# Optimization experiments

Measured on AMD Instinct MI355X. Metric: run time of the kernel, lower is better.

Reference implementation:

```python
import jax, jax.numpy as jnp
import numpy as np

N_NODES = 20000
N_EDGES = 320000
L = 128
NODE_IN = 30
EDGE_IN = 4
NUM_LAYERS = 5


def _mlp(x, w1, b1, a, w2, b2):
    # Linear -> PReLU(scalar slope) -> Linear
    h = x @ w1 + b1
    h = jnp.where(h > 0, h, a * h)
    return h @ w2 + b2


def setup_inputs() -> dict:
    key = jax.random.key(0)
    ks = iter(jax.random.split(key, 64))
    s = 0.02

    def w(shape):
        return (s * jax.random.normal(next(ks), shape)).astype(jnp.float32)

    inp = {}
    inp["x"] = jax.random.normal(next(ks), (N_NODES, NODE_IN), dtype=jnp.float32)
    inp["edge_attr"] = jax.random.normal(next(ks), (N_EDGES, EDGE_IN), dtype=jnp.float32)
    inp["edge_index"] = jax.random.randint(next(ks), (2, N_EDGES), 0, N_NODES, dtype=jnp.int32)
    # node encoder
    inp["ne_w1"] = w((NODE_IN, L)); inp["ne_b1"] = jnp.zeros((L,), jnp.float32)
    inp["ne_a"] = jnp.float32(0.25)
    inp["ne_w2"] = w((L, L)); inp["ne_b2"] = jnp.zeros((L,), jnp.float32)
    # edge encoder
    inp["ee_w1"] = w((EDGE_IN, L)); inp["ee_b1"] = jnp.zeros((L,), jnp.float32)
    inp["ee_a"] = jnp.float32(0.25)
    inp["ee_w2"] = w((L, L)); inp["ee_b2"] = jnp.zeros((L,), jnp.float32)
    # processor layers (stacked over NUM_LAYERS)
    inp["le_w1"] = w((NUM_LAYERS, 3 * L, L)); inp["le_b1"] = jnp.zeros((NUM_LAYERS, L), jnp.float32)
    inp["le_a"] = jnp.full((NUM_LAYERS,), 0.25, jnp.float32)
    inp["le_w2"] = w((NUM_LAYERS, L, L)); inp["le_b2"] = jnp.zeros((NUM_LAYERS, L), jnp.float32)
    inp["ln_w1"] = w((NUM_LAYERS, 2 * L, L)); inp["ln_b1"] = jnp.zeros((NUM_LAYERS, L), jnp.float32)
    inp["ln_a"] = jnp.full((NUM_LAYERS,), 0.25, jnp.float32)
    inp["ln_w2"] = w((NUM_LAYERS, L, L)); inp["ln_b2"] = jnp.zeros((NUM_LAYERS, L), jnp.float32)
    # decoder
    inp["de_w1"] = w((L, L)); inp["de_b1"] = jnp.zeros((L,), jnp.float32)
    inp["de_a"] = jnp.float32(0.25)
    inp["de_w2"] = w((L, 3)); inp["de_b2"] = jnp.zeros((3,), jnp.float32)
    return inp


def reference(x, edge_attr, edge_index,
              ne_w1, ne_b1, ne_a, ne_w2, ne_b2,
              ee_w1, ee_b1, ee_a, ee_w2, ee_b2,
              le_w1, le_b1, le_a, le_w2, le_b2,
              ln_w1, ln_b1, ln_a, ln_w2, ln_b2,
              de_w1, de_b1, de_a, de_w2, de_b2):
    n = x.shape[0]
    src = edge_index[0]  # x_j (source)
    dst = edge_index[1]  # x_i (target), aggregation index

    h = _mlp(x, ne_w1, ne_b1, ne_a, ne_w2, ne_b2)            # [N, L]
    e = _mlp(edge_attr, ee_w1, ee_b1, ee_a, ee_w2, ee_b2)    # [E, L]

    for l in range(le_w1.shape[0]):
        m = jnp.concatenate([h[dst], h[src], e], axis=-1)    # [E, 3L]
        m = _mlp(m, le_w1[l], le_b1[l], le_a[l], le_w2[l], le_b2[l])  # [E, L]
        agg = jax.ops.segment_sum(m, dst, num_segments=n)    # [N, L]
        upd = _mlp(jnp.concatenate([h, agg], axis=-1),
                   ln_w1[l], ln_b1[l], ln_a[l], ln_w2[l], ln_b2[l])
        h = h + upd

    return _mlp(h, de_w1, de_b1, de_a, de_w2, de_b2)         # [N, 3]
```

## Files before the change

### kernel.cpp

```cpp
#include <hip/hip_runtime.h>
#include <cstdint>
#include <cstddef>


#define DEVI static __device__ __forceinline__

typedef __bf16 bf16_t;
typedef bf16_t bf16x8 __attribute__((ext_vector_type(8)));
typedef bf16_t bf16x4 __attribute__((ext_vector_type(4)));
typedef float f32x4v __attribute__((ext_vector_type(4)));

DEVI float4 ld4(const float* p) { return *(const float4*)p; }
DEVI void st4(float* p, float4 v) { *(float4*)p = v; }
DEVI float prelu1(float z, float a) { return z > 0.f ? z : a * z; }
DEVI void atomicAddF(float* p, float v) {
  __hip_atomic_fetch_add(p, v, __ATOMIC_RELAXED, __HIP_MEMORY_SCOPE_AGENT);
}
DEVI f32x4v mfma_bf16(bf16x8 a, bf16x8 b, f32x4v c) {
  return __builtin_amdgcn_mfma_f32_16x16x32_bf16(a, b, c, 0, 0, 0);
}
DEVI void mfma3(f32x4v& acc, bf16x8 ah, bf16x8 al, bf16x8 bh, bf16x8 bl) {
  acc = mfma_bf16(ah, bh, acc);
  acc = mfma_bf16(al, bh, acc);
  acc = mfma_bf16(ah, bl, acc);
}
DEVI void split2(float x, bf16_t& h, bf16_t& l) {
  h = (bf16_t)x;
  l = (bf16_t)(x - (float)h);
}
DEVI bf16x8 ldb8(const bf16_t* p) { return *(const bf16x8*)p; }

#define NST 136
#define EST 72


DEVI void stage_f32(const float* __restrict__ src, int row0, int M,
                    int lane, int wave, bf16_t* SAh, bf16_t* SAl)
{
  const int row = wave * 16 + (lane >> 2);
  const int grow = row0 + row;
  const int colbase = (lane & 3) * 32;
  #pragma unroll
  for (int j = 0; j < 8; ++j) {
    int kc = colbase + j * 4;
    float4 v = make_float4(0.f, 0.f, 0.f, 0.f);
    if (grow < M) v = ld4(src + (size_t)grow * 128 + kc);
    bf16_t h0,l0,h1,l1,h2,l2,h3,l3;
    split2(v.x,h0,l0); split2(v.y,h1,l1); split2(v.z,h2,l2); split2(v.w,h3,l3);
    *(bf16x4*)(SAh + row * NST + kc) = (bf16x4){h0,h1,h2,h3};
    *(bf16x4*)(SAl + row * NST + kc) = (bf16x4){l0,l1,l2,l3};
  }
}

DEVI void stage_planes(const bf16_t* __restrict__ gh, const bf16_t* __restrict__ gl,
                       int row0, int M, int lane, int wave,
                       bf16_t* SAh, bf16_t* SAl)
{
  const int row = wave * 16 + (lane >> 2);
  const int grow = row0 + row;
  const int colbase = (lane & 3) * 32;
  #pragma unroll
  for (int j = 0; j < 4; ++j) {
    int kc = colbase + j * 8;
    bf16x8 vh = {};
    bf16x8 vl = {};
    if (grow < M) {
      vh = ldb8(gh + (size_t)grow * 128 + kc);
      vl = ldb8(gl + (size_t)grow * 128 + kc);
    }
    *(bf16x8*)(SAh + row * NST + kc) = vh;
    *(bf16x8*)(SAl + row * NST + kc) = vl;
  }
}

DEVI void gemm_lds(const bf16_t* SAh, const bf16_t* SAl,
                   const bf16_t* __restrict__ BT, f32x4v acc[8],
                   int wave, int p, int q)
{
  #pragma unroll
  for (int ks = 0; ks < 4; ++ks) {
    const int k0 = ks * 32 + q * 8;
    bf16x8 aH = ldb8(SAh + (wave * 16 + p) * NST + k0);
    bf16x8 aL = ldb8(SAl + (wave * 16 + p) * NST + k0);
    #pragma unroll
    for (int nt = 0; nt < 8; ++nt) {
      const bf16_t* bp = BT + (size_t)(nt * 16 + p) * 128 + k0;
      mfma3(acc[nt], aH, aL, ldb8(bp), ldb8(bp + 16384));
    }
  }
}

DEVI void store_c(float* __restrict__ O, int row0, int M,
                  const f32x4v acc[8], int wave, int p, int q)
{
  int rb = row0 + wave * 16 + q * 4;
  #pragma unroll
  for (int r = 0; r < 4; ++r) {
    if (rb + r < M) {
      float* op = O + (size_t)(rb + r) * 128 + p * 8;
      st4(op,     make_float4(acc[0][r], acc[1][r], acc[2][r], acc[3][r]));
      st4(op + 4, make_float4(acc[4][r], acc[5][r], acc[6][r], acc[7][r]));
    }
  }
}

DEVI void stage_cregs(const f32x4v acc[8], int wave, int p, int q,
                      bf16_t* SAh, bf16_t* SAl)
{
  #pragma unroll
  for (int r = 0; r < 4; ++r) {
    int row = wave * 16 + q * 4 + r;
    bf16x8 vh, vl;
    #pragma unroll
    for (int nt = 0; nt < 8; ++nt) {
      bf16_t hb, lb;
      split2(acc[nt][r], hb, lb);
      vh[nt] = hb; vl[nt] = lb;
    }
    *(bf16x8*)(SAh + row * NST + p * 8) = vh;
    *(bf16x8*)(SAl + row * NST + p * 8) = vl;
  }
}

DEVI void planes_out(bf16_t* __restrict__ gh, bf16_t* __restrict__ gl,
                     int row0, int M, int lane, int wave,
                     const bf16_t* SAh, const bf16_t* SAl)
{
  const int row = wave * 16 + (lane >> 2);
  const int grow = row0 + row;
  const int colbase = (lane & 3) * 32;
  if (grow < M) {
    #pragma unroll
    for (int j = 0; j < 4; ++j) {
      int kc = colbase + j * 8;
      *(bf16x8*)(gh + (size_t)grow * 128 + kc) = *(const bf16x8*)(SAh + row * NST + kc);
      *(bf16x8*)(gl + (size_t)grow * 128 + kc) = *(const bf16x8*)(SAl + row * NST + kc);
    }
  }
}

DEVI void ld8f(float dst[8], const float* __restrict__ src, int p) {
  *(float4*)(dst)     = ld4(src + p * 8);
  *(float4*)(dst + 4) = ld4(src + p * 8 + 4);
}

__global__ __launch_bounds__(128, 2) void k_svu(
    float* Sbuf,
    bf16_t* __restrict__ hSh, bf16_t* __restrict__ hSl,
    const bf16_t* __restrict__ WtilT, const bf16_t* __restrict__ Wn1aT,
    const bf16_t* __restrict__ lnw2T, const bf16_t* __restrict__ W1nextT,
    const float* __restrict__ ln_b1_l, const float* __restrict__ btil_l,
    const int* __restrict__ deg, const float* __restrict__ ln_a_l,
    const float* __restrict__ ln_b2_l,
    float* __restrict__ P, float* __restrict__ Q, int doPQ, int M)
{
  __shared__ __align__(16) bf16_t SAh[32 * NST];
  __shared__ __align__(16) bf16_t SAl[32 * NST];
  const int t = threadIdx.x, lane = t & 63, wave = t >> 6;
  const int p = lane & 15, q = lane >> 4;
  const int row0 = blockIdx.x * 32;

  f32x4v acc1[8];
  #pragma unroll
  for (int j = 0; j < 8; ++j) acc1[j] = (f32x4v){0.f, 0.f, 0.f, 0.f};

  stage_f32(Sbuf, row0, M, lane, wave, SAh, SAl);
  {
    const int row = wave * 16 + (lane >> 2);
    const int grow = row0 + row;
    const int colbase = (lane & 3) * 32;
    if (grow < M) {
      float4 z4 = make_float4(0.f, 0.f, 0.f, 0.f);
      #pragma unroll
      for (int j = 0; j < 8; ++j)
        st4(Sbuf + (size_t)grow * 128 + colbase + j * 4, z4);
    }
  }
  gemm_lds(SAh, SAl, WtilT, acc1, wave, p, q);
  stage_planes(hSh, hSl, row0, M, lane, wave, SAh, SAl);
  gemm_lds(SAh, SAl, Wn1aT, acc1, wave, p, q);

  float hold[8][4];
  #pragma unroll
  for (int r = 0; r < 4; ++r) {
    int row = wave * 16 + q * 4 + r;
    bf16x8 vh = *(const bf16x8*)(SAh + row * NST + p * 8);
    bf16x8 vl = *(const bf16x8*)(SAl + row * NST + p * 8);
    #pragma unroll
    for (int nt = 0; nt < 8; ++nt)
      hold[nt][r] = (float)vh[nt] + (float)vl[nt];
  }
  const float alpha = *ln_a_l;
  float degf[4];
  #pragma unroll
  for (int r = 0; r < 4; ++r) {
    int row = row0 + wave * 16 + q * 4 + r;
    degf[r] = (row < M) ? (float)deg[row] : 0.f;
  }
  float b1c[8], btc[8];
  ld8f(b1c, ln_b1_l, p);
  ld8f(btc, btil_l, p);
  #pragma unroll
  for (int nt = 0; nt < 8; ++nt)
    #pragma unroll
    for (int r = 0; r < 4; ++r)
      acc1[nt][r] = prelu1(acc1[nt][r] + b1c[nt] + degf[r] * btc[nt], alpha);

  stage_cregs(acc1, wave, p, q, SAh, SAl);
  f32x4v acc2[8];
  #pragma unroll
  for (int j = 0; j < 8; ++j) acc2[j] = (f32x4v){0.f, 0.f, 0.f, 0.f};
  gemm_lds(SAh, SAl, lnw2T, acc2, wave, p, q);
  float b2c[8];
  ld8f(b2c, ln_b2_l, p);
  #pragma unroll
  for (int nt = 0; nt < 8; ++nt)
    #pragma unroll
    for (int r = 0; r < 4; ++r)
      acc2[nt][r] = hold[nt][r] + acc2[nt][r] + b2c[nt];

  stage_cregs(acc2, wave, p, q, SAh, SAl);
  planes_out(hSh, hSl, row0, M, lane, wave, SAh, SAl);

  if (doPQ) {
    f32x4v acc3[8];
    #pragma unroll
    for (int j = 0; j < 8; ++j) acc3[j] = (f32x4v){0.f, 0.f, 0.f, 0.f};
    gemm_lds(SAh, SAl, W1nextT, acc3, wave, p, q);
    store_c(P, row0, M, acc3, wave, p, q);
    #pragma unroll
    for (int j = 0; j < 8; ++j) acc3[j] = (f32x4v){0.f, 0.f, 0.f, 0.f};
    gemm_lds(SAh, SAl, W1nextT + 32768, acc3, wave, p, q);
    store_c(Q, row0, M, acc3, wave, p, q);
  }
}

__global__ __launch_bounds__(128, 2) void k_enc(
    const float* __restrict__ UN, const bf16_t* __restrict__ new2T,
    const float* __restrict__ b2, const bf16_t* __restrict__ W1T0,
    bf16_t* __restrict__ hSh, bf16_t* __restrict__ hSl,
    float* __restrict__ P, float* __restrict__ Q, int M)
{
  __shared__ __align__(16) bf16_t SAh[32 * NST];
  __shared__ __align__(16) bf16_t SAl[32 * NST];
  const int t = threadIdx.x, lane = t & 63, wave = t >> 6;
  const int p = lane & 15, q = lane >> 4;
  const int row0 = blockIdx.x * 32;

  f32x4v acc[8];
  #pragma unroll
  for (int j = 0; j < 8; ++j) acc[j] = (f32x4v){0.f, 0.f, 0.f, 0.f};
  stage_f32(UN, row0, M, lane, wave, SAh, SAl);
  gemm_lds(SAh, SAl, new2T, acc, wave, p, q);
  float b2c[8];
  ld8f(b2c, b2, p);
  #pragma unroll
  for (int nt = 0; nt < 8; ++nt)
    #pragma unroll
    for (int r = 0; r < 4; ++r) acc[nt][r] += b2c[nt];
  stage_cregs(acc, wave, p, q, SAh, SAl);
  planes_out(hSh, hSl, row0, M, lane, wave, SAh, SAl);

  f32x4v acc3[8];
  #pragma unroll
  for (int j = 0; j < 8; ++j) acc3[j] = (f32x4v){0.f, 0.f, 0.f, 0.f};
  gemm_lds(SAh, SAl, W1T0, acc3, wave, p, q);
  store_c(P, row0, M, acc3, wave, p, q);
  #pragma unroll
  for (int j = 0; j < 8; ++j) acc3[j] = (f32x4v){0.f, 0.f, 0.f, 0.f};
  gemm_lds(SAh, SAl, W1T0 + 32768, acc3, wave, p, q);
  store_c(Q, row0, M, acc3, wave, p, q);
}

__global__ __launch_bounds__(256, 3) void k_edge(
    const float* __restrict__ sEa, const int* __restrict__ sSrc,
    const int* __restrict__ sDst,
    const int* __restrict__ rowStart, const int* __restrict__ deg,
    const float* __restrict__ ee_w1, const float* __restrict__ ee_b1,
    const float* __restrict__ ee_a,
    const bf16_t* __restrict__ WhatT, const float* __restrict__ bvec,
    const float* __restrict__ alpha_ptr,
    const float* __restrict__ P, const float* __restrict__ Q,
    float* __restrict__ S, int N, int E)
{
  __shared__ __align__(16) float Stile[32 * 132];
  __shared__ __align__(16) float ew[640];
  __shared__ __align__(16) bf16_t Ast[128 * EST];

  const int t = threadIdx.x, lane = t & 63, wave = t >> 6;
  const int p = lane & 15, q = lane >> 4;
  const int e0 = blockIdx.x * 128;
  const int dstLo = sDst[e0];

  const int ebase = e0 + wave * 32 + q * 4;
  int d_[8], s_[8];
  #pragma unroll
  for (int i = 0; i < 8; ++i) {
    int ed = ebase + (i >> 2) * 16 + (i & 3);
    if (ed >= E) ed = E - 1;
    d_[i] = sDst[ed];
    s_[i] = sSrc[ed];
  }

  for (int i = t; i < 640; i += 256)
    ew[i] = (i < 512) ? ee_w1[i] : ee_b1[i - 512];
  for (int i = t; i < 32 * 132; i += 256) Stile[i] = 0.f;
  __syncthreads();

  float q0v[8], q1v[8], q2v[8], q3v[8], pvf[8];
  ld8f(q0v, Q + (size_t)s_[0] * 128, p);
  ld8f(q1v, Q + (size_t)s_[1] * 128, p);
  ld8f(q2v, Q + (size_t)s_[2] * 128, p);
  ld8f(q3v, Q + (size_t)s_[3] * 128, p);
  ld8f(pvf, P + (size_t)d_[0] * 128, p);

  const float ua = *ee_a;
  const float alpha = *alpha_ptr;
  float bvc[8];
  ld8f(bvc, bvec, p);

  const int srow = wave * 32 + (lane >> 1);
  const int scb = (lane & 1) * 32;
  float4 eav = make_float4(0.f, 0.f, 0.f, 0.f);
  {
    int ed = e0 + srow;
    if (ed < E) eav = ld4(sEa + (size_t)ed * 4);
  }

  f32x4v acc[2][8];
  #pragma unroll
  for (int i = 0; i < 2; ++i)
    #pragma unroll
    for (int j = 0; j < 8; ++j) acc[i][j] = (f32x4v){0.f, 0.f, 0.f, 0.f};

  for (int c = 0; c < 2; ++c) {
    #pragma unroll
    for (int j = 0; j < 8; ++j) {
      int kc = scb + j * 4;
      int kg = c * 64 + kc;
      float4 w0 = ld4(ew + kg);
      float4 w1 = ld4(ew + 128 + kg);
      float4 w2 = ld4(ew + 256 + kg);
      float4 w3 = ld4(ew + 384 + kg);
      float4 bb = ld4(ew + 512 + kg);
      float ux = bb.x, uy = bb.y, uz = bb.z, uw = bb.w;
      ux = fmaf(eav.x, w0.x, ux); uy = fmaf(eav.x, w0.y, uy);
      uz = fmaf(eav.x, w0.z, uz); uw = fmaf(eav.x, w0.w, uw);
      ux = fmaf(eav.y, w1.x, ux); uy = fmaf(eav.y, w1.y, uy);
      uz = fmaf(eav.y, w1.z, uz); uw = fmaf(eav.y, w1.w, uw);
      ux = fmaf(eav.z, w2.x, ux); uy = fmaf(eav.z, w2.y, uy);
      uz = fmaf(eav.z, w2.z, uz); uw = fmaf(eav.z, w2.w, uw);
      ux = fmaf(eav.w, w3.x, ux); uy = fmaf(eav.w, w3.y, uy);
      uz = fmaf(eav.w, w3.z, uz); uw = fmaf(eav.w, w3.w, uw);
      *(bf16x4*)(Ast + srow * EST + kc) = (bf16x4){
          (bf16_t)prelu1(ux, ua), (bf16_t)prelu1(uy, ua),
          (bf16_t)prelu1(uz, ua), (bf16_t)prelu1(uw, ua)};
    }
    #pragma unroll
    for (int ks = 0; ks < 2; ++ks) {
      const int k0 = ks * 32 + q * 8;
      const int kg = c * 64 + k0;
      bf16x8 aH0 = ldb8(Ast + (wave * 32 + p) * EST + k0);
      bf16x8 aH1 = ldb8(Ast + (wave * 32 + 16 + p) * EST + k0);
      #pragma unroll
      for (int nt = 0; nt < 8; ++nt) {
        const bf16_t* bp = WhatT + (size_t)(nt * 16 + p) * 128 + kg;
        bf16x8 bH = ldb8(bp);
        bf16x8 bL = ldb8(bp + 16384);
        acc[0][nt] = mfma_bf16(aH0, bH, acc[0][nt]);
        acc[0][nt] = mfma_bf16(aH0, bL, acc[0][nt]);
        acc[1][nt] = mfma_bf16(aH1, bH, acc[1][nt]);
        acc[1][nt] = mfma_bf16(aH1, bL, acc[1][nt]);
      }
    }
  }

  float rs[8];
  #pragma unroll
  for (int nt = 0; nt < 8; ++nt) rs[nt] = 0.f;
  int curd = -1;
  float pv[8];

  #define FLUSH_RS()                                                        \
    if (curd >= 0) {                                                        \
      int rr = curd - dstLo;                                                \
      if (rr < 32) {                                                        \
        _Pragma("unroll")                                                   \
        for (int nt = 0; nt < 8; ++nt)                                      \
          atomicAdd(&Stile[rr * 132 + p * 8 + nt], rs[nt]);                 \
      } else {                                                              \
        _Pragma("unroll")                                                   \
        for (int nt = 0; nt < 8; ++nt)                                      \
          atomicAddF(S + (size_t)curd * 128 + p * 8 + nt, rs[nt]);          \
      }                                                                     \
      _Pragma("unroll")                                                     \
      for (int nt = 0; nt < 8; ++nt) rs[nt] = 0.f;                          \
    }

  #define EDGE_STEP(i, QQ, MT, R)                                           \
    if (ebase + (MT) * 16 + (R) < E) {                                      \
      int d = d_[i];                                                        \
      if (d != curd) {                                                      \
        FLUSH_RS();                                                         \
        curd = d;                                                           \
        ld8f(pv, P + (size_t)d * 128, p);                                   \
        _Pragma("unroll")                                                   \
        for (int nt = 0; nt < 8; ++nt) pv[nt] += bvc[nt];                   \
      }                                                                     \
      _Pragma("unroll")                                                     \
      for (int nt = 0; nt < 8; ++nt)                                        \
        rs[nt] += prelu1(acc[MT][nt][R] + pv[nt] + QQ[nt], alpha);          \
    }

  if (ebase < E) {
    curd = d_[0];
    #pragma unroll
    for (int nt = 0; nt < 8; ++nt) pv[nt] = pvf[nt] + bvc[nt];
    #pragma unroll
    for (int nt = 0; nt < 8; ++nt)
      rs[nt] += prelu1(acc[0][nt][0] + pv[nt] + q0v[nt], alpha);
  }
  ld8f(q0v, Q + (size_t)s_[4] * 128, p);
  EDGE_STEP(1, q1v, 0, 1)
  ld8f(q1v, Q + (size_t)s_[5] * 128, p);
  EDGE_STEP(2, q2v, 0, 2)
  ld8f(q2v, Q + (size_t)s_[6] * 128, p);
  EDGE_STEP(3, q3v, 0, 3)
  ld8f(q3v, Q + (size_t)s_[7] * 128, p);
  EDGE_STEP(4, q0v, 1, 0)
  EDGE_STEP(5, q1v, 1, 1)
  EDGE_STEP(6, q2v, 1, 2)
  EDGE_STEP(7, q3v, 1, 3)
  FLUSH_RS();

  #undef EDGE_STEP
  #undef FLUSH_RS

  __syncthreads();

  const int lastE = (e0 + 127 < E) ? (e0 + 127) : (E - 1);
  const int dstHi = sDst[lastE];
  const int col4 = (t & 31) * 4;
  #pragma unroll
  for (int rr0 = 0; rr0 < 32; rr0 += 8) {
    int rr = rr0 + (t >> 5);
    int d = dstLo + rr;
    if (d <= dstHi && d < N) {
      float4 v = ld4(&Stile[rr * 132 + col4]);
      bool interior = (rowStart[d] >= e0) && (rowStart[d] + deg[d] <= e0 + 128);
      float* sp = S + (size_t)d * 128 + col4;
      if (interior) {
        st4(sp, v);
      } else {
        atomicAddF(sp + 0, v.x); atomicAddF(sp + 1, v.y);
        atomicAddF(sp + 2, v.z); atomicAddF(sp + 3, v.w);
      }
    }
  }
}

__global__ __launch_bounds__(128, 4) void k_dec(
    const bf16_t* __restrict__ hSh, const bf16_t* __restrict__ hSl,
    const bf16_t* __restrict__ dw1T,
    const float* __restrict__ de_b1, const float* __restrict__ de_a,
    const float* __restrict__ de_w2, const float* __restrict__ de_b2,
    float* __restrict__ out, int M)
{
  __shared__ __align__(16) float Cs[32][132];
  __shared__ __align__(16) float w2s[384];
  const int t = threadIdx.x, lane = t & 63, wave = t >> 6;
  const int p = lane & 15, q = lane >> 4;
  const int row0 = blockIdx.x * 32;
  for (int i = t; i < 384; i += 128) w2s[i] = de_w2[i];

  f32x4v acc[8];
  #pragma unroll
  for (int j = 0; j < 8; ++j) acc[j] = (f32x4v){0.f, 0.f, 0.f, 0.f};
  const size_t ra = (size_t)(row0 + wave * 16 + p) * 128;
  #pragma unroll
  for (int ks = 0; ks < 4; ++ks) {
    const int k0 = ks * 32 + q * 8;
    bf16x8 aH = ldb8(hSh + ra + k0);
    bf16x8 aL = ldb8(hSl + ra + k0);
    #pragma unroll
    for (int nt = 0; nt < 8; ++nt) {
      const bf16_t* bp = dw1T + (size_t)(nt * 16 + p) * 128 + k0;
      mfma3(acc[nt], aH, aL, ldb8(bp), ldb8(bp + 16384));
    }
  }
  const float alpha = *de_a;
  float b1c[8];
  ld8f(b1c, de_b1, p);
  #pragma unroll
  for (int r = 0; r < 4; ++r) {
    int row = wave * 16 + q * 4 + r;
    float* cp = &Cs[row][p * 8];
    st4(cp, make_float4(prelu1(acc[0][r] + b1c[0], alpha),
                        prelu1(acc[1][r] + b1c[1], alpha),
                        prelu1(acc[2][r] + b1c[2], alpha),
                        prelu1(acc[3][r] + b1c[3], alpha)));
    st4(cp + 4, make_float4(prelu1(acc[4][r] + b1c[4], alpha),
                            prelu1(acc[5][r] + b1c[5], alpha),
                            prelu1(acc[6][r] + b1c[6], alpha),
                            prelu1(acc[7][r] + b1c[7], alpha)));
  }
  __syncthreads();
  if (t < 32) {
    float s0 = de_b2[0], s1 = de_b2[1], s2 = de_b2[2];
    for (int k = 0; k < 128; ++k) {
      float vv = Cs[t][k];
      s0 = fmaf(vv, w2s[k * 3 + 0], s0);
      s1 = fmaf(vv, w2s[k * 3 + 1], s1);
      s2 = fmaf(vv, w2s[k * 3 + 2], s2);
    }
    int row = row0 + t;
    if (row < M) {
      out[(size_t)row * 3 + 0] = s0;
      out[(size_t)row * 3 + 1] = s1;
      out[(size_t)row * 3 + 2] = s2;
    }
  }
}

__global__ __launch_bounds__(256) void k_tsplit(
    const float* __restrict__ ne_w2, const float* __restrict__ de_w1,
    const float* __restrict__ le_w1, const float* __restrict__ ln_w1,
    const float* __restrict__ ln_w2, bf16_t* __restrict__ WT)
{
  int jid = blockIdx.x;
  const float* src; int slot;
  if (jid == 0)      { src = ne_w2; slot = 0; }
  else if (jid == 1) { src = de_w1; slot = 1; }
  else {
    int l = (jid - 2) >> 2, wj = (jid - 2) & 3;
    slot = 2 + l * 6 + wj;
    src = (wj == 0) ? le_w1 + (size_t)l * 49152
        : (wj == 1) ? le_w1 + (size_t)l * 49152 + 16384
        : (wj == 2) ? ln_w1 + (size_t)l * 32768
                    : ln_w2 + (size_t)l * 16384;
  }
  bf16_t* oh = WT + (size_t)slot * 32768;
  bf16_t* ol = oh + 16384;
  for (int idx = threadIdx.x; idx < 16384; idx += 256) {
    int k = idx >> 7, n = idx & 127;
    bf16_t hb, lb;
    split2(src[idx], hb, lb);
    int pos = ((n & 7) * 16 + (n >> 3)) * 128 + k;
    oh[pos] = hb;
    ol[pos] = lb;
  }
}

__global__ __launch_bounds__(256) void k_fold(
    const float* __restrict__ ee_w2, const float* __restrict__ ee_b2,
    const float* __restrict__ le_w1, const float* __restrict__ le_b1,
    const float* __restrict__ le_w2, const float* __restrict__ le_b2,
    const float* __restrict__ ln_w1,
    bf16_t* __restrict__ WT, float* __restrict__ bvec, float* __restrict__ btil)
{
  const int l = blockIdx.x;
  const int which = blockIdx.y;
  const int z = blockIdx.z;
  const float* L; const float* Rm; const float* lb; const float* badd;
  int slot; float* bout;
  if (which == 0) {
    L = ee_w2; Rm = le_w1 + (size_t)l * 49152 + 256 * 128;
    lb = ee_b2; badd = le_b1 + l * 128;
    slot = 2 + l * 6 + 4; bout = bvec + l * 128;
  } else {
    L = le_w2 + (size_t)l * 16384; Rm = ln_w1 + (size_t)l * 32768 + 128 * 128;
    lb = le_b2 + l * 128; badd = nullptr;
    slot = 2 + l * 6 + 5; bout = btil + l * 128;
  }
  bf16_t* oh = WT + (size_t)slot * 32768;
  bf16_t* ol = oh + 16384;
  const int t = threadIdx.x;
  const int base = z * 2048;
  for (int eidx = base + t; eidx < base + 2048; eidx += 256) {
    int k = eidx >> 7, n = eidx & 127;
    float a = 0.f;
    for (int d = 0; d < 128; d += 4) {
      float4 lv = ld4(L + k * 128 + d);
      a = fmaf(lv.x, Rm[(d + 0) * 128 + n], a);
      a = fmaf(lv.y, Rm[(d + 1) * 128 + n], a);
      a = fmaf(lv.z, Rm[(d + 2) * 128 + n], a);
      a = fmaf(lv.w, Rm[(d + 3) * 128 + n], a);
    }
    bf16_t hb, lbv;
    split2(a, hb, lbv);
    int pos = ((n & 7) * 16 + (n >> 3)) * 128 + k;
    oh[pos] = hb;
    ol[pos] = lbv;
  }
  if (z == 0 && t < 128) {
    float a = badd ? badd[t] : 0.f;
    for (int d = 0; d < 128; ++d) a = fmaf(lb[d], Rm[d * 128 + t], a);
    bout[t] = a;
  }
}

__global__ __launch_bounds__(256) void k_node_u(
    const float* __restrict__ x, const float* __restrict__ w1,
    const float* __restrict__ b1, const float* __restrict__ a_ptr,
    float* __restrict__ U, int M)
{
  int gid = blockIdx.x * 256 + threadIdx.x;
  int m = gid >> 5;
  if (m >= M) return;
  int nc = (gid & 31) << 2;
  float a = *a_ptr;
  float4 bb = ld4(b1 + nc);
  float z0 = bb.x, z1 = bb.y, z2 = bb.z, z3 = bb.w;
  const float* xr = x + (size_t)m * 30;
  #pragma unroll
  for (int j = 0; j < 30; ++j) {
    float xv = xr[j];
    float4 wv = ld4(w1 + j * 128 + nc);
    z0 = fmaf(xv, wv.x, z0); z1 = fmaf(xv, wv.y, z1);
    z2 = fmaf(xv, wv.z, z2); z3 = fmaf(xv, wv.w, z3);
  }
  st4(U + (size_t)m * 128 + nc,
      make_float4(prelu1(z0, a), prelu1(z1, a), prelu1(z2, a), prelu1(z3, a)));
}

__global__ void k_hist(const int* __restrict__ dstIdx, int* __restrict__ deg, int E) {
  int i = blockIdx.x * 256 + threadIdx.x;
  if (i < E) atomicAdd(deg + dstIdx[i], 1);
}

__global__ __launch_bounds__(1024) void k_scan(
    const int* __restrict__ deg, int* __restrict__ cursor,
    int* __restrict__ rowStart, int N, int per)
{
  __shared__ int part[1024];
  const int t = threadIdx.x;
  const int base = t * per;
  int local = 0;
  for (int i = 0; i < per; ++i) {
    int idx = base + i;
    if (idx < N) local += deg[idx];
  }
  part[t] = local;
  __syncthreads();
  for (int off = 1; off < 1024; off <<= 1) {
    int v = (t >= off) ? part[t - off] : 0;
    __syncthreads();
    part[t] += v;
    __syncthreads();
  }
  int run = (t == 0) ? 0 : part[t - 1];
  for (int i = 0; i < per; ++i) {
    int idx = base + i;
    if (idx < N) {
      cursor[idx] = run;
      rowStart[idx] = run;
      run += deg[idx];
    }
  }
}

__global__ void k_scatter(const int* __restrict__ srcIdx, const int* __restrict__ dstIdx,
                          const float* __restrict__ ea, int* __restrict__ cursor,
                          int* __restrict__ sSrc, int* __restrict__ sDst,
                          float* __restrict__ sEa, int E)
{
  int e = blockIdx.x * 256 + threadIdx.x;
  if (e < E) {
    int d = dstIdx[e];
    int p = atomicAdd(cursor + d, 1);
    sSrc[p] = srcIdx[e];
    sDst[p] = d;
    st4(sEa + (size_t)p * 4, ld4(ea + (size_t)e * 4));
  }
}

extern "C" void kernel_launch(void* const* d_in, const int* in_sizes, int n_in,
                              void* d_out, int out_size, void* d_ws, size_t ws_size,
                              hipStream_t stream)
{
  const float* x     = (const float*)d_in[0];
  const float* ea    = (const float*)d_in[1];
  const int*   ei    = (const int*)  d_in[2];
  const float* ne_w1 = (const float*)d_in[3];
  const float* ne_b1 = (const float*)d_in[4];
  const float* ne_a  = (const float*)d_in[5];
  const float* ne_w2 = (const float*)d_in[6];
  const float* ne_b2 = (const float*)d_in[7];
  const float* ee_w1 = (const float*)d_in[8];
  const float* ee_b1 = (const float*)d_in[9];
  const float* ee_a  = (const float*)d_in[10];
  const float* ee_w2 = (const float*)d_in[11];
  const float* ee_b2 = (const float*)d_in[12];
  const float* le_w1 = (const float*)d_in[13];
  const float* le_b1 = (const float*)d_in[14];
  const float* le_a  = (const float*)d_in[15];
  const float* le_w2 = (const float*)d_in[16];
  const float* le_b2 = (const float*)d_in[17];
  const float* ln_w1 = (const float*)d_in[18];
  const float* ln_b1 = (const float*)d_in[19];
  const float* ln_a  = (const float*)d_in[20];
  const float* ln_w2 = (const float*)d_in[21];
  const float* ln_b2 = (const float*)d_in[22];
  const float* de_w1 = (const float*)d_in[23];
  const float* de_b1 = (const float*)d_in[24];
  const float* de_a  = (const float*)d_in[25];
  const float* de_w2 = (const float*)d_in[26];
  const float* de_b2 = (const float*)d_in[27];

  const int N = in_sizes[0] / 30;
  const int E = in_sizes[1] / 4;
  const int* srcIdx = ei;
  const int* dstIdx = ei + E;

  const int g32 = (N + 31) / 32;
  const int gE  = (E + 127) / 128;
  const int Np = g32 * 32;
  const size_t NNp = (size_t)Np * 128;

  float* w = (float*)d_ws;
  float* Pb   = w; w += NNp;
  float* Qb   = w; w += NNp;
  float* Sb   = w; w += NNp;
  float* bvec = w; w += 5 * 128;
  float* btil = w; w += 5 * 128;
  float* sEa  = w; w += (size_t)E * 4;
  bf16_t* hSh = (bf16_t*)w;
  bf16_t* hSl = hSh + NNp;  w += NNp;
  bf16_t* WT  = (bf16_t*)w; w += 32 * 32768 / 2;
  int* ip     = (int*)w;
  int* deg    = ip; ip += N;
  int* cursor = ip; ip += N;
  int* rowStart = ip; ip += N;
  int* sSrc   = ip; ip += E;
  int* sDst   = ip; ip += E;

  float* out = (float*)d_out;

  k_tsplit<<<dim3(22), dim3(256), 0, stream>>>(ne_w2, de_w1, le_w1, ln_w1, ln_w2, WT);
  k_fold<<<dim3(5, 2, 8), dim3(256), 0, stream>>>(ee_w2, ee_b2, le_w1, le_b1,
                                                  le_w2, le_b2, ln_w1, WT, bvec, btil);
  hipMemsetAsync(deg, 0, (size_t)N * 4, stream);
  k_hist<<<dim3((E + 255) / 256), dim3(256), 0, stream>>>(dstIdx, deg, E);
  k_scan<<<dim3(1), dim3(1024), 0, stream>>>(deg, cursor, rowStart, N,
                                             (N + 1023) / 1024);
  k_scatter<<<dim3((E + 255) / 256), dim3(256), 0, stream>>>(
      srcIdx, dstIdx, ea, cursor, sSrc, sDst, sEa, E);

  k_node_u<<<dim3((N * 32 + 255) / 256), dim3(256), 0, stream>>>(x, ne_w1, ne_b1, ne_a, Sb, N);
  k_enc<<<dim3(g32), dim3(128), 0, stream>>>(Sb, WT, ne_b2, WT + 2 * 32768,
                                             hSh, hSl, Pb, Qb, N);

  hipMemsetAsync(Sb, 0, (size_t)N * 128 * 4, stream);

  for (int l = 0; l < 5; ++l) {
    const bf16_t* slotL = WT + (size_t)(2 + l * 6) * 32768;
    k_edge<<<dim3(gE), dim3(256), 0, stream>>>(
        sEa, sSrc, sDst, rowStart, deg, ee_w1, ee_b1, ee_a,
        slotL + 4 * 32768, bvec + l * 128, le_a + l, Pb, Qb, Sb, N, E);
    const bf16_t* W1next = (l < 4) ? (WT + (size_t)(2 + (l + 1) * 6) * 32768) : WT;
    k_svu<<<dim3(g32), dim3(128), 0, stream>>>(
        Sb, hSh, hSl, slotL + 5 * 32768, slotL + 2 * 32768, slotL + 3 * 32768,
        W1next, ln_b1 + (size_t)l * 128, btil + l * 128, deg, ln_a + l,
        ln_b2 + (size_t)l * 128, Pb, Qb, (l < 4) ? 1 : 0, N);
  }

  k_dec<<<dim3(g32), dim3(128), 0, stream>>>(hSh, hSl, WT + 32768, de_b1, de_a,
                                             de_w2, de_b2, out, N);
}
```

Baseline: 1.432 ms.

## Gather Q source rows into LDS via global_load_lds in edge kernel

Replaces per-lane register gathers of Q[src] rows with direct global-to-LDS async loads (global_load_lds, 16 bytes per lane), staged in two halves of 16 edges per wave, reusing the LDS region formerly used for the A tile. Each half is waited on with vmcnt(0) and then read from LDS in the epilogue. The goal is coalesced full-row gathers with lower VGPR pressure. In exchange it adds LDS traffic, an extra barrier and full-drain waits that limit overlap. Shared memory per block also grows from about 18KB to 32KB for that buffer, which may affect occupancy at 3 blocks per CU.

```diff
diff --git a/kernel.cpp b/kernel.cpp
--- a/kernel.cpp
+++ b/kernel.cpp
@@ -29,6 +29,12 @@
   l = (bf16_t)(x - (float)h);
 }
 DEVI bf16x8 ldb8(const bf16_t* p) { return *(const bf16x8*)p; }
+
+typedef const __attribute__((address_space(1))) unsigned int* gas_u32;
+typedef __attribute__((address_space(3))) unsigned int* las_u32;
+DEVI void gld_lds16(const float* g, void* l) {
+  __builtin_amdgcn_global_load_lds((gas_u32)g, (las_u32)l, 16, 0, 0);
+}
 
 #define NST 136
 #define EST 72
@@ -285,34 +291,35 @@
 {
   __shared__ __align__(16) float Stile[32 * 132];
   __shared__ __align__(16) float ew[640];
-  __shared__ __align__(16) bf16_t Ast[128 * EST];
+  __shared__ __align__(16) char QSmem[32768];
+  bf16_t* Ast = (bf16_t*)QSmem;
 
   const int t = threadIdx.x, lane = t & 63, wave = t >> 6;
   const int p = lane & 15, q = lane >> 4;
   const int e0 = blockIdx.x * 128;
   const int dstLo = sDst[e0];
-
   const int ebase = e0 + wave * 32 + q * 4;
-  int d_[8], s_[8];
+
+  int d_[8];
   #pragma unroll
   for (int i = 0; i < 8; ++i) {
     int ed = ebase + (i >> 2) * 16 + (i & 3);
-    if (ed >= E) ed = E - 1;
-    d_[i] = sDst[ed];
-    s_[i] = sSrc[ed];
-  }
+    d_[i] = sDst[ed < E ? ed : E - 1];
+  }
+  const int sbase = e0 + wave * 32 + (lane >> 5);
+  int sv0[8];
+  #pragma unroll
+  for (int k = 0; k < 8; ++k) {
+    int ed = sbase + 2 * k;
+    sv0[k] = sSrc[ed < E ? ed : E - 1];
+  }
+  float pvf[8];
+  ld8f(pvf, P + (size_t)d_[0] * 128, p);
 
   for (int i = t; i < 640; i += 256)
     ew[i] = (i < 512) ? ee_w1[i] : ee_b1[i - 512];
   for (int i = t; i < 32 * 132; i += 256) Stile[i] = 0.f;
   __syncthreads();
-
-  float q0v[8], q1v[8], q2v[8], q3v[8], pvf[8];
-  ld8f(q0v, Q + (size_t)s_[0] * 128, p);
-  ld8f(q1v, Q + (size_t)s_[1] * 128, p);
-  ld8f(q2v, Q + (size_t)s_[2] * 128, p);
-  ld8f(q3v, Q + (size_t)s_[3] * 128, p);
-  ld8f(pvf, P + (size_t)d_[0] * 128, p);
 
   const float ua = *ee_a;
   const float alpha = *alpha_ptr;
@@ -375,11 +382,33 @@
     }
   }
 
+  __syncthreads();
+
+  char* qbase = QSmem + wave * 8192;
+  const int cw = (lane & 31) * 4;
+  #pragma unroll
+  for (int k = 0; k < 8; ++k)
+    gld_lds16(Q + (size_t)sv0[k] * 128 + cw, qbase + k * 1024);
+  int sv1[8];
+  #pragma unroll
+  for (int k = 0; k < 8; ++k) {
+    int ed = sbase + 16 + 2 * k;
+    sv1[k] = sSrc[ed < E ? ed : E - 1];
+  }
+  asm volatile("s_waitcnt vmcnt(0)" ::: "memory");
+
+  const float* qw = (const float*)QSmem + wave * 2048;
+
   float rs[8];
   #pragma unroll
   for (int nt = 0; nt < 8; ++nt) rs[nt] = 0.f;
   int curd = -1;
   float pv[8];
+  if (ebase < E) {
+    curd = d_[0];
+    #pragma unroll
+    for (int nt = 0; nt < 8; ++nt) pv[nt] = pvf[nt] + bvc[nt];
+  }
 
   #define FLUSH_RS()                                                        \
     if (curd >= 0) {                                                        \
@@ -397,9 +426,9 @@
       for (int nt = 0; nt < 8; ++nt) rs[nt] = 0.f;                          \
     }
 
-  #define EDGE_STEP(i, QQ, MT, R)                                           \
+  #define QEDGE(MT, R)                                                      \
     if (ebase + (MT) * 16 + (R) < E) {                                      \
-      int d = d_[i];                                                        \
+      int d = d_[(MT) * 4 + (R)];                                           \
       if (d != curd) {                                                      \
         FLUSH_RS();                                                         \
         curd = d;                                                           \
@@ -407,33 +436,36 @@
         _Pragma("unroll")                                                   \
         for (int nt = 0; nt < 8; ++nt) pv[nt] += bvc[nt];                   \
       }                                                                     \
-      _Pragma("unroll")                                                     \
-      for (int nt = 0; nt < 8; ++nt)                                        \
-        rs[nt] += prelu1(acc[MT][nt][R] + pv[nt] + QQ[nt], alpha);          \
-    }
-
-  if (ebase < E) {
-    curd = d_[0];
-    #pragma unroll
-    for (int nt = 0; nt < 8; ++nt) pv[nt] = pvf[nt] + bvc[nt];
-    #pragma unroll
-    for (int nt = 0; nt < 8; ++nt)
-      rs[nt] += prelu1(acc[0][nt][0] + pv[nt] + q0v[nt], alpha);
-  }
-  ld8f(q0v, Q + (size_t)s_[4] * 128, p);
-  EDGE_STEP(1, q1v, 0, 1)
-  ld8f(q1v, Q + (size_t)s_[5] * 128, p);
-  EDGE_STEP(2, q2v, 0, 2)
-  ld8f(q2v, Q + (size_t)s_[6] * 128, p);
-  EDGE_STEP(3, q3v, 0, 3)
-  ld8f(q3v, Q + (size_t)s_[7] * 128, p);
-  EDGE_STEP(4, q0v, 1, 0)
-  EDGE_STEP(5, q1v, 1, 1)
-  EDGE_STEP(6, q2v, 1, 2)
-  EDGE_STEP(7, q3v, 1, 3)
+      const float* qr = qw + (q * 4 + (R)) * 128 + p * 8;                   \
+      float4 qa = ld4(qr);                                                  \
+      float4 qb = ld4(qr + 4);                                              \
+      rs[0] += prelu1(acc[MT][0][(R)] + pv[0] + qa.x, alpha);               \
+      rs[1] += prelu1(acc[MT][1][(R)] + pv[1] + qa.y, alpha);               \
+      rs[2] += prelu1(acc[MT][2][(R)] + pv[2] + qa.z, alpha);               \
+      rs[3] += prelu1(acc[MT][3][(R)] + pv[3] + qa.w, alpha);               \
+      rs[4] += prelu1(acc[MT][4][(R)] + pv[4] + qb.x, alpha);               \
+      rs[5] += prelu1(acc[MT][5][(R)] + pv[5] + qb.y, alpha);               \
+      rs[6] += prelu1(acc[MT][6][(R)] + pv[6] + qb.z, alpha);               \
+      rs[7] += prelu1(acc[MT][7][(R)] + pv[7] + qb.w, alpha);               \
+    }
+
+  QEDGE(0, 0)
+  QEDGE(0, 1)
+  QEDGE(0, 2)
+  QEDGE(0, 3)
+
+  #pragma unroll
+  for (int k = 0; k < 8; ++k)
+    gld_lds16(Q + (size_t)sv1[k] * 128 + cw, qbase + k * 1024);
+  asm volatile("s_waitcnt vmcnt(0)" ::: "memory");
+
+  QEDGE(1, 0)
+  QEDGE(1, 1)
+  QEDGE(1, 2)
+  QEDGE(1, 3)
   FLUSH_RS();
 
-  #undef EDGE_STEP
+  #undef QEDGE
   #undef FLUSH_RS
 
   __syncthreads();
```

New measurement: 1.429 ms. No clear change (-0.3%).
